# Kernel optimization log

Hardware: AMD Instinct MI355X
Metric: run time of the kernel (lower is better)

The kernel has to match this reference:

```python
import jax, jax.numpy as jnp
import numpy as np
from jax import lax

B, T, H, C = 64, 512, 1024, 8


def setup_inputs() -> dict:
    key = jax.random.key(0)
    ks = jax.random.split(key, 7)
    encoding = jax.random.normal(ks[0], (B, T, H), dtype=jnp.float32)
    labels = jax.random.randint(ks[1], (B, 3 * T), 0, C)
    W = jax.random.normal(ks[2], (3, C, H), dtype=jnp.float32) * 0.02
    b = jax.random.normal(ks[3], (3, C), dtype=jnp.float32) * 0.02
    start_trans = jax.random.normal(ks[4], (3, C), dtype=jnp.float32) * 0.1
    end_trans = jax.random.normal(ks[5], (3, C), dtype=jnp.float32) * 0.1
    trans = jax.random.normal(ks[6], (3, C, C), dtype=jnp.float32) * 0.1
    return {"encoding": encoding, "labels": labels, "W": W, "b": b,
            "start_trans": start_trans, "end_trans": end_trans, "trans": trans}


def crf_neg_log_lik(em, tags, start, end, trans):
    # em [B,T,C], tags [B,T] -> scalar (torchcrf reduction='sum', loss = -llh)
    bsz = em.shape[0]
    # numerator: score of gold path
    em_sc = jnp.take_along_axis(em, tags[:, :, None], axis=2)[..., 0].sum(axis=1)
    tr_sc = trans[tags[:, :-1], tags[:, 1:]].sum(axis=1)
    num = start[tags[:, 0]] + em_sc + tr_sc + end[tags[:, -1]]
    # denominator: forward algorithm (log partition)
    a0 = start[None, :] + em[:, 0]  # [B,C]

    def step(a, e_t):
        a_new = jax.nn.logsumexp(a[:, :, None] + trans[None] + e_t[:, None, :], axis=1)
        return a_new, None

    aT, _ = lax.scan(step, a0, jnp.moveaxis(em[:, 1:], 1, 0))
    logZ = jax.nn.logsumexp(aT + end[None, :], axis=1)
    return -(num - logZ).sum()


def viterbi(em, start, end, trans):
    # em [B,T,C] -> best tag path [B,T] (no mask: all sequences full length)
    v0 = start[None, :] + em[:, 0]

    def step(v, e_t):
        s = v[:, :, None] + trans[None]          # [B,C_prev,C_cur]
        bp = jnp.argmax(s, axis=1)               # [B,C]
        return jnp.max(s, axis=1) + e_t, bp

    vT, bps = lax.scan(step, v0, jnp.moveaxis(em[:, 1:], 1, 0))  # bps [T-1,B,C]
    last = jnp.argmax(vT + end[None, :], axis=1)  # [B]

    def back(tag, bp):
        prev = jnp.take_along_axis(bp, tag[:, None], axis=1)[:, 0]
        return prev, prev

    _, rev = lax.scan(back, last, bps, reverse=True)  # [T-1,B], tags for t=0..T-2
    tags = jnp.concatenate([rev, last[None]], axis=0)  # [T,B]
    return tags.T


def reference(encoding, labels, W, b, start_trans, end_trans, trans):
    # three per-task projections: logits [3,B,T,C]
    logits = jnp.einsum('bth,kch->kbtc', encoding, W) + b[:, None, None, :]
    tags = jnp.stack(jnp.split(labels, 3, axis=1))  # [3,B,T] (task/process/material)
    losses = jax.vmap(crf_neg_log_lik)(logits, tags, start_trans, end_trans, trans)
    loss = losses.sum()
    pred = jax.vmap(viterbi)(logits, start_trans, end_trans, trans)  # [3,B,T]
    return loss, logits, pred
```

## Files before the change

kernel.cpp:

```cpp
#include <hip/hip_runtime.h>

#define NB 64
#define NT 512
#define NH 1024
#define NC 8
#define NK 3
#define BT (NB*NT)
#define LOGITS_N (NK*BT*NC)

#define QP1  0xB1
#define QP2  0x4E
#define ROR4 0x124
#define ROR8 0x128
#define HM   0x141

template<int CTRL>
__device__ __forceinline__ float dppf(float x) {
  return __int_as_float(__builtin_amdgcn_update_dpp(0, __float_as_int(x), CTRL, 0xF, 0xF, true));
}
template<int CTRL>
__device__ __forceinline__ int dppi(int x) {
  return __builtin_amdgcn_update_dpp(0, x, CTRL, 0xF, 0xF, true);
}

__device__ __forceinline__ void gload_lds16(const float* g, float* l) {
  __builtin_amdgcn_global_load_lds(
      (const __attribute__((address_space(1))) void*)g,
      (__attribute__((address_space(3))) void*)l, 16, 0, 0);
}

__global__ __launch_bounds__(256) void init_kernel(const float* __restrict__ W,
                                                   float* __restrict__ Wt,
                                                   float* __restrict__ out) {
  int i = blockIdx.x * 256 + threadIdx.x;
  if (i < 24 * NH) {
    int h = i / 24, j = i - h * 24;
    int kk = j >> 3, cc = j & 7;
    Wt[i] = W[kk * NC * NH + cc * NH + h];
  }
  if (i == 0) out[0] = 0.0f;
}

__global__ __launch_bounds__(512, 1) void proj_kernel(const float* __restrict__ enc,
                                                      const float* __restrict__ Wt,
                                                      const float* __restrict__ bias,
                                                      float* __restrict__ out) {
  __shared__ float smem[25600];
  const int tid = threadIdx.x;
  const int lane = tid & 63;
  const int w = tid >> 6;
  const int row0 = blockIdx.x * 128;
  const float* eb = enc + (size_t)row0 * 1024;

  float acc0[24], acc1[24];
#pragma unroll
  for (int j = 0; j < 24; ++j) { acc0[j] = 0.0f; acc1[j] = 0.0f; }

  auto stage = [&](int ci, int buf) {
#pragma unroll
    for (int i = 0; i < 4; ++i) {
      const int rbase = w * 16 + i * 4;
      const int r = rbase + (lane >> 4);
      const int s = (lane & 15) ^ (r & 7);
      gload_lds16(eb + (size_t)r * 1024 + ci * 64 + s * 4,
                  &smem[buf * 8192 + rbase * 64]);
    }
  };

  auto compute = [&](int ci, int buf) {
    const float* wp = Wt + __builtin_amdgcn_readfirstlane((ci * 64 + w * 8) * 24);
    const int sw = lane & 7;
    const float* r0 = &smem[buf * 8192 + lane * 64];
    const float* r1 = r0 + 4096;
#pragma unroll
    for (int t = 0; t < 2; ++t) {
      const int sl = (((w * 2 + t) ^ sw)) * 4;
      const float4 e0 = *(const float4*)&r0[sl];
      const float4 e1 = *(const float4*)&r1[sl];
      const float ev0[4] = {e0.x, e0.y, e0.z, e0.w};
      const float ev1[4] = {e1.x, e1.y, e1.z, e1.w};
      const float* wt4 = wp + t * 96;
#pragma unroll
      for (int m = 0; m < 4; ++m) {
        const float a = ev0[m], b = ev1[m];
        const float* wc = wt4 + m * 24;
#pragma unroll
        for (int j = 0; j < 24; ++j) {
          acc0[j] = fmaf(a, wc[j], acc0[j]);
          acc1[j] = fmaf(b, wc[j], acc1[j]);
        }
      }
    }
  };

  stage(0, 0);

#pragma unroll 1
  for (int ci = 0; ci < 16; ++ci) {
    const int buf = ci & 1;
    __syncthreads();
    if (ci < 15) stage(ci + 1, buf ^ 1);
    compute(ci, buf);
  }

  __syncthreads();
  {
    float* p0 = &smem[w * 3200 + lane * 25];
    float* p1 = p0 + 64 * 25;
#pragma unroll
    for (int j = 0; j < 24; ++j) { p0[j] = acc0[j]; p1[j] = acc1[j]; }
  }
  __syncthreads();
  {
    const int row = tid >> 2, j0 = (tid & 3) * 6;
#pragma unroll
    for (int u = 0; u < 6; ++u) {
      const int j = j0 + u;
      float s = bias[j];
#pragma unroll
      for (int w8 = 0; w8 < 8; ++w8) s += smem[w8 * 3200 + row * 25 + j];
      out[1 + (size_t)(j >> 3) * (BT * 8) + (size_t)(row0 + row) * 8 + (j & 7)] = s;
    }
  }
}

__global__ __launch_bounds__(512) void crf_kernel(const int* __restrict__ labels,
                                                  const float* __restrict__ startT,
                                                  const float* __restrict__ endT,
                                                  const float* __restrict__ trans,
                                                  float* __restrict__ d_out) {
  __shared__ float sA[32 * 64];
  __shared__ float sVB[32 * 8];
  __shared__ int   sBP[512];
  __shared__ int   sMap[32 * 8];
  __shared__ int   sEnt[32];
  __shared__ float sRed[32];
  __shared__ unsigned char sTags[512];
  __shared__ int sTerm;

  const int tid = threadIdx.x;
  const int lane = tid & 63;
  const int w = tid >> 6;
  const int c = lane & 7;
  const int p = (lane >> 3) & 7;
  const int role = (blockIdx.x >= 192);
  const int seq = role ? blockIdx.x - 192 : blockIdx.x;
  const int k = seq >> 6, b = seq & 63;
  const float* em = d_out + 1 + ((size_t)k * BT + (size_t)b * 512) * 8;
  const float* trk = trans + k * 64;
  const int* lab = labels + b * (NK * NT) + k * NT;

  float Txc[8];
#pragma unroll
  for (int kk = 0; kk < 8; ++kk) Txc[kk] = trk[(c ^ kk) * 8 + c];
  const float Tpc = trk[p * 8 + c];
  const float startc = startT[k * 8 + c];
  const float endc = endT[k * 8 + c];

  if (!role) {
    float Mxc[8];
#pragma unroll
    for (int kk = 0; kk < 8; ++kk) Mxc[kk] = __expf(Txc[kk]);

#pragma unroll 1
    for (int it = 0; it < 4; ++it) {
      const int i = w * 4 + it;
      const int t0 = i * 16;
      const int te = (t0 + 16 < 512) ? (t0 + 16) : 511;
      float EX[16];
      EX[0] = em[(t0 + 1) * 8 + c];
#pragma unroll
      for (int j = 1; j < 16; ++j) {
        int t = t0 + 1 + j;
        EX[j] = (t <= te) ? __expf(em[t * 8 + c]) : 1.0f;
      }
      float V = __expf(Tpc + EX[0]);
#pragma unroll
      for (int j = 1; j < 16; ++j) {
        int t = t0 + 1 + j;
        if (t <= te) {
          float x1 = dppf<QP1>(V), x2 = dppf<QP2>(V), x3 = dppf<QP2>(x1);
          float x7 = dppf<HM>(V), x6 = dppf<QP1>(x7), x5 = dppf<QP2>(x7), x4 = dppf<QP2>(x6);
          float s01 = fmaf(x1, Mxc[1], V * Mxc[0]);
          float s23 = fmaf(x3, Mxc[3], x2 * Mxc[2]);
          float s45 = fmaf(x5, Mxc[5], x4 * Mxc[4]);
          float s67 = fmaf(x7, Mxc[7], x6 * Mxc[6]);
          V = ((s01 + s23) + (s45 + s67)) * EX[j];
        }
        if (j == 8) V *= 0x1p-32f;
      }
      sA[i * 64 + lane] = V;
    }
    __syncthreads();

    float logZ = 0.0f;
    if (w == 0) {
      float al = __expf(startc + em[c]);
      float lz = 0.0f;
#pragma unroll 1
      for (int i = 0; i < 32; ++i) {
        const float* Ai = &sA[i * 64];
        float A0 = Ai[(c ^ 0) * 8 + c], A1 = Ai[(c ^ 1) * 8 + c];
        float A2 = Ai[(c ^ 2) * 8 + c], A3 = Ai[(c ^ 3) * 8 + c];
        float A4 = Ai[(c ^ 4) * 8 + c], A5 = Ai[(c ^ 5) * 8 + c];
        float A6 = Ai[(c ^ 6) * 8 + c], A7 = Ai[(c ^ 7) * 8 + c];
        float a1 = dppf<QP1>(al), a2 = dppf<QP2>(al), a3 = dppf<QP2>(a1);
        float a4 = dppf<ROR4>(al), a5 = dppf<ROR4>(a1), a6 = dppf<ROR4>(a2), a7 = dppf<ROR4>(a3);
        float s01 = fmaf(a1, A1, al * A0);
        float s23 = fmaf(a3, A3, a2 * A2);
        float s45 = fmaf(a5, A5, a4 * A4);
        float s67 = fmaf(a7, A7, a6 * A6);
        float s = (s01 + s23) + (s45 + s67);
        float ss = s;
        ss += dppf<QP1>(ss); ss += dppf<QP2>(ss); ss += dppf<ROR4>(ss);
        lz += __logf(ss);
        al = s * (1.0f / ss);
      }
      float se = al * __expf(endc);
      se += dppf<QP1>(se); se += dppf<QP2>(se); se += dppf<ROR4>(se);
      logZ = lz + __logf(se) + 1024.0f * 0.69314718055994531f;
    } else {
      int idx = (w - 1) * 64 + lane;
      float ns = 0.0f;
      {
        int tg = lab[idx];
        ns += em[(size_t)idx * 8 + tg] + trk[tg * 8 + lab[idx + 1]];
      }
      if (idx < 64) {
        int t = idx + 448;
        int tg = lab[t];
        ns += em[(size_t)t * 8 + tg];
        if (t < 511) ns += trk[tg * 8 + lab[t + 1]];
      }
      ns += dppf<QP1>(ns); ns += dppf<QP2>(ns); ns += dppf<HM>(ns); ns += dppf<ROR8>(ns);
      if ((lane & 15) == 0) sRed[(w - 1) * 4 + (lane >> 4)] = ns;
    }
    __syncthreads();
    if (tid == 0) {
      float num = startT[k * 8 + lab[0]] + endT[k * 8 + lab[511]];
#pragma unroll
      for (int u = 0; u < 28; ++u) num += sRed[u];
      atomicAdd(d_out, logZ - num);
    }
  } else {
#pragma unroll 1
    for (int it = 0; it < 4; ++it) {
      const int i = w * 4 + it;
      const int t0 = i * 16;
      const int te = (t0 + 16 < 512) ? (t0 + 16) : 511;
      float emv[16];
#pragma unroll
      for (int j = 0; j < 16; ++j) {
        int t = t0 + 1 + j;
        emv[j] = (t <= te) ? em[t * 8 + c] : 0.0f;
      }
      float V = Tpc + emv[0];
#pragma unroll
      for (int j = 1; j < 16; ++j) {
        int t = t0 + 1 + j;
        if (t <= te) {
          float x1 = dppf<QP1>(V), x2 = dppf<QP2>(V), x3 = dppf<QP2>(x1);
          float x7 = dppf<HM>(V), x6 = dppf<QP1>(x7), x5 = dppf<QP2>(x7), x4 = dppf<QP2>(x6);
          float c0 = V + Txc[0], c1 = x1 + Txc[1], c2 = x2 + Txc[2], c3 = x3 + Txc[3];
          float c4 = x4 + Txc[4], c5 = x5 + Txc[5], c6 = x6 + Txc[6], c7 = x7 + Txc[7];
          float m0 = fmaxf(fmaxf(c0, c1), c2);
          float m1 = fmaxf(fmaxf(c3, c4), c5);
          float m2 = fmaxf(c6, c7);
          V = fmaxf(fmaxf(m0, m1), m2) + emv[j];
        }
      }
      sA[i * 64 + lane] = V;
    }
    __syncthreads();

    if (w == 0) {
      float v = startc + em[c];
#pragma unroll 1
      for (int i = 0; i < 32; ++i) {
        if (lane < 8) sVB[i * 8 + c] = v;
        const float* Ai = &sA[i * 64];
        float A0 = Ai[(c ^ 0) * 8 + c], A1 = Ai[(c ^ 1) * 8 + c];
        float A2 = Ai[(c ^ 2) * 8 + c], A3 = Ai[(c ^ 3) * 8 + c];
        float A4 = Ai[(c ^ 4) * 8 + c], A5 = Ai[(c ^ 5) * 8 + c];
        float A6 = Ai[(c ^ 6) * 8 + c], A7 = Ai[(c ^ 7) * 8 + c];
        float a1 = dppf<QP1>(v), a2 = dppf<QP2>(v), a3 = dppf<QP2>(a1);
        float a4 = dppf<ROR4>(v), a5 = dppf<ROR4>(a1), a6 = dppf<ROR4>(a2), a7 = dppf<ROR4>(a3);
        float c0 = v + A0, c1 = a1 + A1, c2 = a2 + A2, c3 = a3 + A3;
        float c4 = a4 + A4, c5 = a5 + A5, c6 = a6 + A6, c7 = a7 + A7;
        float m0 = fmaxf(fmaxf(c0, c1), c2);
        float m1 = fmaxf(fmaxf(c3, c4), c5);
        float m2 = fmaxf(c6, c7);
        v = fmaxf(fmaxf(m0, m1), m2);
      }
      float lv = v + endc;
      int li = c;
      {
        float ov; int oi; bool take;
        ov = dppf<QP1>(lv); oi = dppi<QP1>(li);
        take = (ov > lv) || (ov == lv && oi < li); lv = take ? ov : lv; li = take ? oi : li;
        ov = dppf<QP2>(lv); oi = dppi<QP2>(li);
        take = (ov > lv) || (ov == lv && oi < li); lv = take ? ov : lv; li = take ? oi : li;
        ov = dppf<ROR4>(lv); oi = dppi<ROR4>(li);
        take = (ov > lv) || (ov == lv && oi < li); lv = take ? ov : lv; li = take ? oi : li;
      }
      if (lane == 0) sTerm = li;
    }
    __syncthreads();

    if (w < 4) {
      const int u = lane >> 3;
      const int i = w * 8 + u;
      const int t0 = i * 16;
      const int te = (t0 + 16 < 512) ? (t0 + 16) : 511;
      float emv[16];
#pragma unroll
      for (int j = 0; j < 16; ++j) {
        int t = t0 + 1 + j;
        emv[j] = (t <= te) ? em[t * 8 + c] : 0.0f;
      }
      float v = sVB[i * 8 + c];
#pragma unroll
      for (int j = 0; j < 16; ++j) {
        int t = t0 + 1 + j;
        if (t <= te) {
          float x1 = dppf<QP1>(v), x2 = dppf<QP2>(v), x3 = dppf<QP2>(x1);
          float x7 = dppf<HM>(v), x6 = dppf<QP1>(x7), x5 = dppf<QP2>(x7), x4 = dppf<QP2>(x6);
          float c0 = v + Txc[0], c1 = x1 + Txc[1], c2 = x2 + Txc[2], c3 = x3 + Txc[3];
          float c4 = x4 + Txc[4], c5 = x5 + Txc[5], c6 = x6 + Txc[6], c7 = x7 + Txc[7];
          float m0 = fmaxf(fmaxf(c0, c1), c2);
          float m1 = fmaxf(fmaxf(c3, c4), c5);
          float m2 = fmaxf(c6, c7);
          float best = fmaxf(fmaxf(m0, m1), m2);
          int a0 = (c0 == best) ? (c ^ 0) : 8;
          int a1i = (c1 == best) ? (c ^ 1) : 8;
          int a2i = (c2 == best) ? (c ^ 2) : 8;
          int a3i = (c3 == best) ? (c ^ 3) : 8;
          int a4i = (c4 == best) ? (c ^ 4) : 8;
          int a5i = (c5 == best) ? (c ^ 5) : 8;
          int a6i = (c6 == best) ? (c ^ 6) : 8;
          int a7i = (c7 == best) ? (c ^ 7) : 8;
          int arg = min(min(min(a0, a1i), min(a2i, a3i)),
                        min(min(a4i, a5i), min(a6i, a7i)));
          v = best + emv[j];
          int wd = arg << (3 * c);
          wd |= dppi<QP1>(wd); wd |= dppi<QP2>(wd); wd |= dppi<HM>(wd);
          if ((lane & 7) == 0) sBP[t] = wd;
        }
      }
    }
    __syncthreads();

    if (w < 4) {
      const int u = lane >> 3;
      const int i = w * 8 + u;
      const int t0 = i * 16;
      const int te = (t0 + 16 < 512) ? (t0 + 16) : 511;
      int tag = c;
#pragma unroll
      for (int j = 16; j >= 1; --j) {
        int t = t0 + j;
        if (t <= te) tag = (sBP[t] >> (3 * tag)) & 7;
      }
      sMap[i * 8 + c] = tag;
    }
    __syncthreads();
    if (tid == 0) {
      int cur = sTerm;
#pragma unroll 1
      for (int i = 31; i >= 0; --i) { cur = sMap[i * 8 + cur]; sEnt[i] = cur; }
    }
    __syncthreads();
    if (w == 0 && lane < 32) {
      const int i = lane;
      const int t0 = i * 16;
      const int te = (t0 + 16 < 512) ? (t0 + 16) : 511;
      int tag = (i == 31) ? sTerm : sEnt[i + 1];
      if (i == 31) sTags[511] = (unsigned char)tag;
#pragma unroll
      for (int j = 16; j >= 1; --j) {
        int t = t0 + j;
        if (t <= te) { tag = (sBP[t] >> (3 * tag)) & 7; sTags[t - 1] = (unsigned char)tag; }
      }
    }
    __syncthreads();
    float* outp = d_out + 1 + LOGITS_N + (size_t)seq * 512;
    outp[tid] = (float)sTags[tid];
  }
}

extern "C" void kernel_launch(void* const* d_in, const int* in_sizes, int n_in,
                              void* d_out, int out_size, void* d_ws, size_t ws_size,
                              hipStream_t stream) {
  const float* enc    = (const float*)d_in[0];
  const int*   labels = (const int*)  d_in[1];
  const float* W      = (const float*)d_in[2];
  const float* bias   = (const float*)d_in[3];
  const float* startT = (const float*)d_in[4];
  const float* endT   = (const float*)d_in[5];
  const float* trans  = (const float*)d_in[6];
  float* out = (float*)d_out;
  float* Wt  = (float*)d_ws;

  init_kernel<<<dim3(96), dim3(256), 0, stream>>>(W, Wt, out);
  proj_kernel<<<dim3(256), dim3(512), 0, stream>>>(enc, Wt, bias, out);
  crf_kernel<<<dim3(384), dim3(512), 0, stream>>>(labels, startT, endT, trans, out);
}
```

Baseline: 251.7 us.

## Stage full projection weights in LDS and halve the encoding chunk size

Loads the whole transposed weight matrix (24x1024 floats) into shared memory once per block instead of reading it from global/scalar memory each chunk. The encoding staging chunk shrinks from 64 to 32 columns, doubling the iteration count, and the barrier moves to the end of each iteration. This is meant to cut repeated global weight traffic and scalar-load latency, but it raises LDS use to 128 KB and adds LDS vector reads for the weights.

```diff
diff --git a/kernel.cpp b/kernel.cpp
--- a/kernel.cpp
+++ b/kernel.cpp
@@ -45,7 +45,9 @@
                                                       const float* __restrict__ Wt,
                                                       const float* __restrict__ bias,
                                                       float* __restrict__ out) {
-  __shared__ float smem[25600];
+  __shared__ float smem[32768];
+  float* const sW = smem;
+  float* const sStage = smem + 24576;
   const int tid = threadIdx.x;
   const int lane = tid & 63;
   const int w = tid >> 6;
@@ -56,54 +58,60 @@
 #pragma unroll
   for (int j = 0; j < 24; ++j) { acc0[j] = 0.0f; acc1[j] = 0.0f; }
 
+#pragma unroll
+  for (int i = 0; i < 12; ++i) {
+    const int u = w * 12 + i;
+    gload_lds16(Wt + u * 256 + lane * 4, &sW[u * 256]);
+  }
+
   auto stage = [&](int ci, int buf) {
 #pragma unroll
-    for (int i = 0; i < 4; ++i) {
-      const int rbase = w * 16 + i * 4;
-      const int r = rbase + (lane >> 4);
-      const int s = (lane & 15) ^ (r & 7);
-      gload_lds16(eb + (size_t)r * 1024 + ci * 64 + s * 4,
-                  &smem[buf * 8192 + rbase * 64]);
+    for (int i = 0; i < 2; ++i) {
+      const int rbase = w * 16 + i * 8;
+      const int r = rbase + (lane >> 3);
+      const int s = (lane & 7) ^ (r & 7);
+      gload_lds16(eb + (size_t)r * 1024 + ci * 32 + s * 4,
+                  &sStage[buf * 4096 + rbase * 32]);
     }
   };
 
   auto compute = [&](int ci, int buf) {
-    const float* wp = Wt + __builtin_amdgcn_readfirstlane((ci * 64 + w * 8) * 24);
-    const int sw = lane & 7;
-    const float* r0 = &smem[buf * 8192 + lane * 64];
-    const float* r1 = r0 + 4096;
-#pragma unroll
-    for (int t = 0; t < 2; ++t) {
-      const int sl = (((w * 2 + t) ^ sw)) * 4;
-      const float4 e0 = *(const float4*)&r0[sl];
-      const float4 e1 = *(const float4*)&r1[sl];
-      const float ev0[4] = {e0.x, e0.y, e0.z, e0.w};
-      const float ev1[4] = {e1.x, e1.y, e1.z, e1.w};
-      const float* wt4 = wp + t * 96;
-#pragma unroll
-      for (int m = 0; m < 4; ++m) {
-        const float a = ev0[m], b = ev1[m];
-        const float* wc = wt4 + m * 24;
-#pragma unroll
-        for (int j = 0; j < 24; ++j) {
-          acc0[j] = fmaf(a, wc[j], acc0[j]);
-          acc1[j] = fmaf(b, wc[j], acc1[j]);
-        }
+    const float* wp = &sW[(ci * 32 + w * 4) * 24];
+    const int sl = (w ^ (lane & 7)) * 4;
+    const float* r0 = &sStage[buf * 4096 + lane * 32];
+    const float4 e0 = *(const float4*)&r0[sl];
+    const float4 e1 = *(const float4*)&r0[64 * 32 + sl];
+    const float ev0[4] = {e0.x, e0.y, e0.z, e0.w};
+    const float ev1[4] = {e1.x, e1.y, e1.z, e1.w};
+#pragma unroll
+    for (int h = 0; h < 4; ++h) {
+      const float* wh = wp + h * 24;
+      float wv[24];
+#pragma unroll
+      for (int q = 0; q < 6; ++q) {
+        const float4 t4 = *(const float4*)&wh[q * 4];
+        wv[q*4+0] = t4.x; wv[q*4+1] = t4.y; wv[q*4+2] = t4.z; wv[q*4+3] = t4.w;
+      }
+      const float a = ev0[h], b = ev1[h];
+#pragma unroll
+      for (int j = 0; j < 24; ++j) {
+        acc0[j] = fmaf(a, wv[j], acc0[j]);
+        acc1[j] = fmaf(b, wv[j], acc1[j]);
       }
     }
   };
 
   stage(0, 0);
-
-#pragma unroll 1
-  for (int ci = 0; ci < 16; ++ci) {
+  __syncthreads();
+
+#pragma unroll 1
+  for (int ci = 0; ci < 32; ++ci) {
     const int buf = ci & 1;
-    __syncthreads();
-    if (ci < 15) stage(ci + 1, buf ^ 1);
+    if (ci < 31) stage(ci + 1, buf ^ 1);
     compute(ci, buf);
-  }
-
-  __syncthreads();
+    __syncthreads();
+  }
+
   {
     float* p0 = &smem[w * 3200 + lane * 25];
     float* p1 = p0 + 64 * 25;
```

Result: faster. 241.8 us (-3.9%).

## Compute projection with split-bf16 MFMA instead of scalar FP32 FMAs

Applied to the files above, without the earlier changes.

The encoder projection GEMM moves from per-thread scalar FMAs to 16x16x32 bf16 MFMA instructions. FP32 accuracy is emulated by splitting both operands into three bf16 parts and accumulating six cross products. The weights are pre-split and laid out in MFMA fragment order by the init kernel, and the cross-wave LDS reduction in the epilogue is removed. Each wave now owns 16 rows over the full K range, which adds per-element splitting work on the activations and a small accuracy risk from the dropped low-order terms.

```diff
diff --git a/kernel.cpp b/kernel.cpp
--- a/kernel.cpp
+++ b/kernel.cpp
@@ -8,6 +8,12 @@
 #define BT (NB*NT)
 #define LOGITS_N (NK*BT*NC)
 
+typedef unsigned short ushort;
+typedef unsigned int uint;
+typedef __attribute__((ext_vector_type(8))) short short8v;
+typedef __attribute__((ext_vector_type(4))) float float4v;
+union S8 { short8v v; ushort u[8]; };
+
 #define QP1  0xB1
 #define QP2  0x4E
 #define ROR4 0x124
@@ -23,103 +29,145 @@
   return __builtin_amdgcn_update_dpp(0, x, CTRL, 0xF, 0xF, true);
 }
 
-__device__ __forceinline__ void gload_lds16(const float* g, float* l) {
+__device__ __forceinline__ void gload_lds16(const void* g, void* l) {
   __builtin_amdgcn_global_load_lds(
       (const __attribute__((address_space(1))) void*)g,
       (__attribute__((address_space(3))) void*)l, 16, 0, 0);
 }
 
 __global__ __launch_bounds__(256) void init_kernel(const float* __restrict__ W,
-                                                   float* __restrict__ Wt,
+                                                   ushort* __restrict__ WB,
                                                    float* __restrict__ out) {
-  int i = blockIdx.x * 256 + threadIdx.x;
-  if (i < 24 * NH) {
-    int h = i / 24, j = i - h * 24;
-    int kk = j >> 3, cc = j & 7;
-    Wt[i] = W[kk * NC * NH + cc * NH + h];
-  }
+  const int i = blockIdx.x * 256 + threadIdx.x;
+  const int ci = i >> 11;
+  const int rem = i & 2047;
+  const int q = rem >> 9;
+  const int l = (rem >> 3) & 63;
+  const int e = i & 7;
+  const int k = ci * 64 + (q >> 1) * 32 + ((l >> 4) << 3) + e;
+  const int j = (q & 1) * 16 + (l & 15);
+  float v = 0.0f;
+  if (j < 24) v = W[(j >> 3) * (NC * NH) + (j & 7) * NH + k];
+  const uint b = __float_as_uint(v);
+  const ushort h1 = (ushort)(b >> 16);
+  const float f1 = __uint_as_float(b & 0xFFFF0000u);
+  const float r1 = v - f1;
+  const uint b2 = __float_as_uint(r1);
+  const ushort h2 = (ushort)(b2 >> 16);
+  const float f2 = __uint_as_float(b2 & 0xFFFF0000u);
+  const float r2 = r1 - f2;
+  const ushort h3 = (ushort)(__float_as_uint(r2) >> 16);
+  WB[i] = h1;
+  WB[32768 + i] = h2;
+  WB[65536 + i] = h3;
   if (i == 0) out[0] = 0.0f;
 }
 
-__global__ __launch_bounds__(512, 1) void proj_kernel(const float* __restrict__ enc,
-                                                      const float* __restrict__ Wt,
+__global__ __launch_bounds__(512, 2) void proj_kernel(const float* __restrict__ enc,
+                                                      const ushort* __restrict__ WB,
                                                       const float* __restrict__ bias,
                                                       float* __restrict__ out) {
-  __shared__ float smem[25600];
+  __shared__ float  sA[2][8192];
+  __shared__ ushort sB[2][6144];
   const int tid = threadIdx.x;
   const int lane = tid & 63;
   const int w = tid >> 6;
   const int row0 = blockIdx.x * 128;
   const float* eb = enc + (size_t)row0 * 1024;
 
-  float acc0[24], acc1[24];
-#pragma unroll
-  for (int j = 0; j < 24; ++j) { acc0[j] = 0.0f; acc1[j] = 0.0f; }
-
-  auto stage = [&](int ci, int buf) {
+  float4v acc0 = {0.0f, 0.0f, 0.0f, 0.0f};
+  float4v acc1 = {0.0f, 0.0f, 0.0f, 0.0f};
+
+  auto stageA = [&](int ci, int buf) {
 #pragma unroll
     for (int i = 0; i < 4; ++i) {
       const int rbase = w * 16 + i * 4;
       const int r = rbase + (lane >> 4);
-      const int s = (lane & 15) ^ (r & 7);
-      gload_lds16(eb + (size_t)r * 1024 + ci * 64 + s * 4,
-                  &smem[buf * 8192 + rbase * 64]);
+      const int s = (lane & 15) ^ (r & 15);
+      gload_lds16(eb + (size_t)r * 1024 + ci * 64 + s * 4, &sA[buf][rbase * 64]);
     }
   };
-
-  auto compute = [&](int ci, int buf) {
-    const float* wp = Wt + __builtin_amdgcn_readfirstlane((ci * 64 + w * 8) * 24);
-    const int sw = lane & 7;
-    const float* r0 = &smem[buf * 8192 + lane * 64];
-    const float* r1 = r0 + 4096;
-#pragma unroll
-    for (int t = 0; t < 2; ++t) {
-      const int sl = (((w * 2 + t) ^ sw)) * 4;
-      const float4 e0 = *(const float4*)&r0[sl];
-      const float4 e1 = *(const float4*)&r1[sl];
-      const float ev0[4] = {e0.x, e0.y, e0.z, e0.w};
-      const float ev1[4] = {e1.x, e1.y, e1.z, e1.w};
-      const float* wt4 = wp + t * 96;
-#pragma unroll
-      for (int m = 0; m < 4; ++m) {
-        const float a = ev0[m], b = ev1[m];
-        const float* wc = wt4 + m * 24;
-#pragma unroll
-        for (int j = 0; j < 24; ++j) {
-          acc0[j] = fmaf(a, wc[j], acc0[j]);
-          acc1[j] = fmaf(b, wc[j], acc1[j]);
-        }
-      }
+  auto stageB = [&](int ci, int buf) {
+    {
+      const int u = w;
+      gload_lds16(WB + (u >> 2) * 32768 + ci * 2048 + (u & 3) * 512 + lane * 8,
+                  &sB[buf][u * 512]);
+    }
+    if (w < 4) {
+      const int u = 8 + w;
+      gload_lds16(WB + (u >> 2) * 32768 + ci * 2048 + (u & 3) * 512 + lane * 8,
+                  &sB[buf][u * 512]);
     }
   };
 
-  stage(0, 0);
+  auto compute = [&](int buf) {
+    const float* ar = &sA[buf][(w * 16 + (lane & 15)) * 64];
+    const ushort* sBf = &sB[buf][0];
+    const int rx = lane & 15;
+    const int g = lane >> 4;
+#pragma unroll
+    for (int kkb = 0; kkb < 2; ++kkb) {
+      const int s0 = kkb * 8 + g * 2;
+      const float4 e0 = *(const float4*)&ar[(s0 ^ rx) * 4];
+      const float4 e1 = *(const float4*)&ar[((s0 + 1) ^ rx) * 4];
+      S8 a1, a2, a3;
+      const float vals[8] = {e0.x, e0.y, e0.z, e0.w, e1.x, e1.y, e1.z, e1.w};
+#pragma unroll
+      for (int t = 0; t < 8; ++t) {
+        const float v = vals[t];
+        const uint b = __float_as_uint(v);
+        a1.u[t] = (ushort)(b >> 16);
+        const float f1 = __uint_as_float(b & 0xFFFF0000u);
+        const float r1 = v - f1;
+        const uint b2 = __float_as_uint(r1);
+        a2.u[t] = (ushort)(b2 >> 16);
+        const float f2 = __uint_as_float(b2 & 0xFFFF0000u);
+        const float r2 = r1 - f2;
+        a3.u[t] = (ushort)(__float_as_uint(r2) >> 16);
+      }
+#pragma unroll
+      for (int jt = 0; jt < 2; ++jt) {
+        const int q = kkb * 2 + jt;
+        const short8v w1 = *(const short8v*)&sBf[0 * 2048 + q * 512 + lane * 8];
+        const short8v w2 = *(const short8v*)&sBf[1 * 2048 + q * 512 + lane * 8];
+        const short8v w3 = *(const short8v*)&sBf[2 * 2048 + q * 512 + lane * 8];
+        float4v acc = jt ? acc1 : acc0;
+        acc = __builtin_amdgcn_mfma_f32_16x16x32_bf16(a1.v, w1, acc, 0, 0, 0);
+        acc = __builtin_amdgcn_mfma_f32_16x16x32_bf16(a2.v, w1, acc, 0, 0, 0);
+        acc = __builtin_amdgcn_mfma_f32_16x16x32_bf16(a1.v, w2, acc, 0, 0, 0);
+        acc = __builtin_amdgcn_mfma_f32_16x16x32_bf16(a2.v, w2, acc, 0, 0, 0);
+        acc = __builtin_amdgcn_mfma_f32_16x16x32_bf16(a3.v, w1, acc, 0, 0, 0);
+        acc = __builtin_amdgcn_mfma_f32_16x16x32_bf16(a1.v, w3, acc, 0, 0, 0);
+        if (jt) acc1 = acc; else acc0 = acc;
+      }
+    }
+  };
+
+  stageA(0, 0);
+  stageB(0, 0);
+  __syncthreads();
 
 #pragma unroll 1
   for (int ci = 0; ci < 16; ++ci) {
     const int buf = ci & 1;
-    __syncthreads();
-    if (ci < 15) stage(ci + 1, buf ^ 1);
-    compute(ci, buf);
+    if (ci < 15) { stageA(ci + 1, buf ^ 1); stageB(ci + 1, buf ^ 1); }
+    compute(buf);
+    __syncthreads();
   }
 
-  __syncthreads();
-  {
-    float* p0 = &smem[w * 3200 + lane * 25];
-    float* p1 = p0 + 64 * 25;
-#pragma unroll
-    for (int j = 0; j < 24; ++j) { p0[j] = acc0[j]; p1[j] = acc1[j]; }
-  }
-  __syncthreads();
-  {
-    const int row = tid >> 2, j0 = (tid & 3) * 6;
-#pragma unroll
-    for (int u = 0; u < 6; ++u) {
-      const int j = j0 + u;
-      float s = bias[j];
-#pragma unroll
-      for (int w8 = 0; w8 < 8; ++w8) s += smem[w8 * 3200 + row * 25 + j];
-      out[1 + (size_t)(j >> 3) * (BT * 8) + (size_t)(row0 + row) * 8 + (j & 7)] = s;
+  const int g = lane >> 4, cx = lane & 15;
+#pragma unroll
+  for (int jt = 0; jt < 2; ++jt) {
+    const int j = jt * 16 + cx;
+    if (j < 24) {
+      const float bj = bias[j];
+      const float4v acc = jt ? acc1 : acc0;
+      float* ob = out + 1 + (size_t)(j >> 3) * (BT * 8) + (j & 7);
+#pragma unroll
+      for (int qq = 0; qq < 4; ++qq) {
+        const int grow = row0 + w * 16 + g * 4 + qq;
+        ob[(size_t)grow * 8] = acc[qq] + bj;
+      }
     }
   }
 }
@@ -399,9 +447,9 @@
   const float* endT   = (const float*)d_in[5];
   const float* trans  = (const float*)d_in[6];
   float* out = (float*)d_out;
-  float* Wt  = (float*)d_ws;
-
-  init_kernel<<<dim3(96), dim3(256), 0, stream>>>(W, Wt, out);
-  proj_kernel<<<dim3(256), dim3(512), 0, stream>>>(enc, Wt, bias, out);
+  ushort* WB = (ushort*)d_ws;
+
+  init_kernel<<<dim3(128), dim3(256), 0, stream>>>(W, WB, out);
+  proj_kernel<<<dim3(256), dim3(512), 0, stream>>>(enc, WB, bias, out);
   crf_kernel<<<dim3(384), dim3(512), 0, stream>>>(labels, startT, endT, trans, out);
 }
```

Measured after the change: 238.8 us. -5.1%, faster.
